# Optimization experiments

Hardware: AMD Instinct MI355X
Metric: run time of the kernel (lower is better)

The kernel has to match this reference:

```python
import jax, jax.numpy as jnp
import numpy as np

B, S, D = 32, 128, 512       # batch, seq_len, input_dim
UNITS = 4096                 # LSTM cell units
PROJ = 512                   # projection_dim
CELL_CLIP = 3.0
PROJ_CLIP = 3.0
W_SCALE = 0.05               # keep gates out of saturation


def hard_sigmoid(x):
    # Keras hard_sigmoid: clip(0.2*x + 0.5, 0, 1)
    return jnp.clip(0.2 * x + 0.5, 0.0, 1.0)


def setup_inputs() -> dict:
    key = jax.random.key(0)
    k = jax.random.split(key, 5)
    x = jax.random.normal(k[0], (B, S, D), dtype=jnp.float32)
    kernel = jax.random.normal(k[1], (D, 4 * UNITS), dtype=jnp.float32) * W_SCALE
    recurrent_kernel = jax.random.normal(k[2], (PROJ, 4 * UNITS), dtype=jnp.float32) * W_SCALE
    bias = jax.random.normal(k[3], (4 * UNITS,), dtype=jnp.float32) * W_SCALE
    # unit_forget_bias: forget-gate slice initialized to ones
    bias = bias.at[UNITS:2 * UNITS].set(1.0)
    projection_kernel = jax.random.normal(k[4], (UNITS, PROJ), dtype=jnp.float32) * W_SCALE
    return {"x": x, "kernel": kernel, "recurrent_kernel": recurrent_kernel,
            "bias": bias, "projection_kernel": projection_kernel}


def reference(x, kernel, recurrent_kernel, bias, projection_kernel):
    # LSTM with cell-state clipping and output projection (ELMo-style).
    # Gate order in fused kernels: [i, f, c, o].
    def step(carry, x_t):
        h, c = carry                              # h: [B,PROJ], c: [B,UNITS]
        z = x_t @ kernel + h @ recurrent_kernel + bias   # [B, 4*UNITS]
        zi, zf, zc, zo = jnp.split(z, 4, axis=-1)
        i = hard_sigmoid(zi)
        f = hard_sigmoid(zf)
        c_new = f * c + i * jnp.tanh(zc)
        o = hard_sigmoid(zo)
        h_new = o * jnp.tanh(c_new)               # uses UNCLIPPED c (matches source)
        c_new = jnp.clip(c_new, -CELL_CLIP, CELL_CLIP)
        h_new = jnp.clip(h_new @ projection_kernel, -PROJ_CLIP, PROJ_CLIP)  # [B,PROJ]
        return (h_new, c_new), h_new

    h0 = jnp.zeros((x.shape[0], PROJ), dtype=x.dtype)
    c0 = jnp.zeros((x.shape[0], UNITS), dtype=x.dtype)
    xs = jnp.transpose(x, (1, 0, 2))              # [S,B,D]
    _, hs = jax.lax.scan(step, (h0, c0), xs)      # hs: [S,B,PROJ]
    return jnp.transpose(hs, (1, 0, 2))           # [B,S,PROJ] (return_sequences)
```

## Files before the change

kernel.cpp:

```cpp
#include <hip/hip_runtime.h>


#define NBLK 256
#define NTHR 512
#define B_   32
#define S_   128
#define D_   512
#define U_   4096
#define PJ   512
#define G4   16384
#define PITC 520
#define LSCALE 2048.0f
#define LINV   4.8828125e-4f

typedef __attribute__((ext_vector_type(8))) _Float16 half8;
typedef __attribute__((ext_vector_type(4))) float floatx4;
typedef __attribute__((ext_vector_type(4))) unsigned int uintx4;

__device__ __forceinline__ void split_h(float f, _Float16& hi, _Float16& lo) {
  _Float16 h = (_Float16)f;
  hi = h;
  lo = (_Float16)((f - (float)h) * LSCALE);
}

__device__ __forceinline__ void stg_dev_u32(unsigned* p, unsigned v) {
  __hip_atomic_store(p, v, __ATOMIC_RELAXED, __HIP_MEMORY_SCOPE_AGENT);
}
__device__ __forceinline__ void store16_sc1(float* p, floatx4 v) {
  asm volatile("global_store_dwordx4 %0, %1, off sc1" :: "v"(p), "v"(v) : "memory");
}
__device__ __forceinline__ uintx4 ld16u_sc1(const unsigned* p) {
  uintx4 r;
  asm volatile("global_load_dwordx4 %0, %1, off sc1\n\ts_waitcnt vmcnt(0)"
               : "=v"(r) : "v"(p) : "memory");
  return r;
}

__global__ __launch_bounds__(NTHR, 2)
void lstm_persistent(const float* __restrict__ x,
                     const float* __restrict__ Wk,
                     const float* __restrict__ R,
                     const float* __restrict__ bias,
                     const float* __restrict__ P,
                     float* __restrict__ out,
                     unsigned* __restrict__ flags1,
                     unsigned* __restrict__ flags2,
                     float* __restrict__ hbuf,
                     float* __restrict__ partial)
{
  __shared__ __align__(16) char smem[100352];
  _Float16* xh_hi = (_Float16*)smem;
  _Float16* xh_lo = xh_hi + B_ * PITC;
  float (*zb)[64][33] = (float (*)[64][33])(smem + 66560);
  float* part_lds = (float*)smem;
  __shared__ float cst[512];
  __shared__ float biasL[64];
  __shared__ _Float16 hph[1024], hpl[1024];
  __shared__ floatx4 redf4[512];

  const int tid  = threadIdx.x;
  const int blk  = blockIdx.x;
  const int lane = tid & 63;
  const int w    = tid >> 6;
  const int ch   = w & 1;
  const int sq   = w >> 1;

  if (tid < 64) {
    int gg = tid >> 4, j = tid & 15;
    biasL[tid] = bias[gg * U_ + blk * 16 + j];
  }
  cst[tid] = 0.f;
  for (int i = tid; i < 1024; i += NTHR) { hph[i] = (_Float16)0.f; hpl[i] = (_Float16)0.f; }

  half8 bhi[2][2][4], blo[2][2][4];
  {
    const int n = lane & 15, q = lane >> 4;
#pragma unroll
    for (int c = 0; c < 2; ++c) {
      const float* Wsrc = c ? R : Wk;
#pragma unroll
      for (int nt = 0; nt < 2; ++nt) {
        int cib  = ch * 32 + nt * 16 + n;
        int gcol = (cib >> 4) * U_ + blk * 16 + (cib & 15);
#pragma unroll
        for (int u = 0; u < 4; ++u) {
          half8 th, tl;
#pragma unroll
          for (int i = 0; i < 8; ++i) {
            int k = (sq * 4 + u) * 32 + q * 8 + i;
            _Float16 hi, lo;
            split_h(Wsrc[(size_t)k * G4 + gcol], hi, lo);
            th[i] = hi; tl[i] = lo;
          }
          bhi[nt][c][u] = th;
          blo[nt][c][u] = tl;
        }
      }
    }
  }

  half8 psh[4], psl[4];
  {
    const int n = lane & 15, q = lane >> 4;
#pragma unroll
    for (int nt = 0; nt < 4; ++nt) {
      half8 th, tl;
#pragma unroll
      for (int i = 0; i < 8; ++i) { th[i] = (_Float16)0.f; tl[i] = (_Float16)0.f; }
      if (q < 2) {
#pragma unroll
        for (int i = 0; i < 8; ++i) {
          int k = q * 8 + i;
          _Float16 hi, lo;
          split_h(P[(size_t)(blk * 16 + k) * PJ + (w * 64 + nt * 16 + n)], hi, lo);
          th[i] = hi; tl[i] = lo;
        }
      }
      psh[nt] = th; psl[nt] = tl;
    }
  }
  __syncthreads();

  const int rb = blk >> 3;
  const int rn = (blk & 7) << 6;
  const int o4 = tid & 15;
  const int gg = tid >> 4;
  const int m_ = lane & 15, q = lane >> 4;

  for (int t = 0; t < S_; ++t) {
    floatx4 acc00 = {0.f, 0.f, 0.f, 0.f};
    floatx4 acc01 = acc00, acc10 = acc00, acc11 = acc00;
    floatx4 accL00 = acc00, accL01 = acc00, accL10 = acc00, accL11 = acc00;

#pragma unroll
    for (int it = 0; it < 4; ++it) {
      int c8 = tid + it * NTHR;
      int b  = c8 >> 6;
      int kg = (c8 & 63) << 3;
      const float* src = x + (size_t)(b * S_ + t) * D_ + kg;
      floatx4 f0 = *(const floatx4*)src;
      floatx4 f1 = *(const floatx4*)(src + 4);
      half8 th, tl; _Float16 hi, lo;
      split_h(f0.x, hi, lo); th[0] = hi; tl[0] = lo;
      split_h(f0.y, hi, lo); th[1] = hi; tl[1] = lo;
      split_h(f0.z, hi, lo); th[2] = hi; tl[2] = lo;
      split_h(f0.w, hi, lo); th[3] = hi; tl[3] = lo;
      split_h(f1.x, hi, lo); th[4] = hi; tl[4] = lo;
      split_h(f1.y, hi, lo); th[5] = hi; tl[5] = lo;
      split_h(f1.z, hi, lo); th[6] = hi; tl[6] = lo;
      split_h(f1.w, hi, lo); th[7] = hi; tl[7] = lo;
      *(half8*)(xh_hi + b * PITC + kg) = th;
      *(half8*)(xh_lo + b * PITC + kg) = tl;
    }
    __syncthreads();

    if (t > 0) {
      const unsigned e = (unsigned)t;
      if (w == 0) {
        for (;;) {
          uintx4 v = ld16u_sc1(flags1 + lane * 4);
          if (__all((int)(v.x >= e && v.y >= e && v.z >= e && v.w >= e))) break;
          __builtin_amdgcn_s_sleep(2);
        }
      }
      __syncthreads();
      {
        const float* pb = partial + (size_t)gg * 16384 + (size_t)rb * PJ + rn + o4 * 4;
        floatx4 r0, r1, r2, r3, r4, r5, r6, r7;
        asm volatile("global_load_dwordx4 %0, %1, off sc1" : "=v"(r0) : "v"(pb)           : "memory");
        asm volatile("global_load_dwordx4 %0, %1, off sc1" : "=v"(r1) : "v"(pb +  524288) : "memory");
        asm volatile("global_load_dwordx4 %0, %1, off sc1" : "=v"(r2) : "v"(pb + 1048576) : "memory");
        asm volatile("global_load_dwordx4 %0, %1, off sc1" : "=v"(r3) : "v"(pb + 1572864) : "memory");
        asm volatile("global_load_dwordx4 %0, %1, off sc1" : "=v"(r4) : "v"(pb + 2097152) : "memory");
        asm volatile("global_load_dwordx4 %0, %1, off sc1" : "=v"(r5) : "v"(pb + 2621440) : "memory");
        asm volatile("global_load_dwordx4 %0, %1, off sc1" : "=v"(r6) : "v"(pb + 3145728) : "memory");
        asm volatile("global_load_dwordx4 %0, %1, off sc1" : "=v"(r7) : "v"(pb + 3670016) : "memory");
        asm volatile("s_waitcnt vmcnt(0)" ::: "memory");
        __builtin_amdgcn_sched_barrier(0);
        floatx4 s = ((r0 + r1) + (r2 + r3)) + ((r4 + r5) + (r6 + r7));
        redf4[gg * 16 + o4] = s;
      }
      __syncthreads();
      if (tid < 16) {
        floatx4 a = redf4[tid];
#pragma unroll
        for (int g2 = 1; g2 < 32; ++g2) a += redf4[g2 * 16 + tid];
        a.x = fminf(fmaxf(a.x, -3.f), 3.f);
        a.y = fminf(fmaxf(a.y, -3.f), 3.f);
        a.z = fminf(fmaxf(a.z, -3.f), 3.f);
        a.w = fminf(fmaxf(a.w, -3.f), 3.f);
        store16_sc1(hbuf + (size_t)t * 16384 + (size_t)rb * PJ + rn + tid * 4, a);
        *(floatx4*)(out + ((size_t)rb * S_ + (t - 1)) * PJ + rn + tid * 4) = a;
      }
      __syncthreads();
      if (tid == 0) stg_dev_u32(flags2 + blk, e);
    }

#pragma unroll
    for (int u = 0; u < 4; ++u) {
      int ko = (sq * 4 + u) * 32 + q * 8;
      half8 ah0 = *(const half8*)(xh_hi + m_ * PITC + ko);
      half8 ah1 = *(const half8*)(xh_hi + (16 + m_) * PITC + ko);
      half8 al0 = *(const half8*)(xh_lo + m_ * PITC + ko);
      half8 al1 = *(const half8*)(xh_lo + (16 + m_) * PITC + ko);
      acc00 = __builtin_amdgcn_mfma_f32_16x16x32_f16(ah0, bhi[0][0][u], acc00, 0, 0, 0);
      acc01 = __builtin_amdgcn_mfma_f32_16x16x32_f16(ah0, bhi[1][0][u], acc01, 0, 0, 0);
      acc10 = __builtin_amdgcn_mfma_f32_16x16x32_f16(ah1, bhi[0][0][u], acc10, 0, 0, 0);
      acc11 = __builtin_amdgcn_mfma_f32_16x16x32_f16(ah1, bhi[1][0][u], acc11, 0, 0, 0);
      accL00 = __builtin_amdgcn_mfma_f32_16x16x32_f16(ah0, blo[0][0][u], accL00, 0, 0, 0);
      accL01 = __builtin_amdgcn_mfma_f32_16x16x32_f16(ah0, blo[1][0][u], accL01, 0, 0, 0);
      accL10 = __builtin_amdgcn_mfma_f32_16x16x32_f16(ah1, blo[0][0][u], accL10, 0, 0, 0);
      accL11 = __builtin_amdgcn_mfma_f32_16x16x32_f16(ah1, blo[1][0][u], accL11, 0, 0, 0);
      accL00 = __builtin_amdgcn_mfma_f32_16x16x32_f16(al0, bhi[0][0][u], accL00, 0, 0, 0);
      accL01 = __builtin_amdgcn_mfma_f32_16x16x32_f16(al0, bhi[1][0][u], accL01, 0, 0, 0);
      accL10 = __builtin_amdgcn_mfma_f32_16x16x32_f16(al1, bhi[0][0][u], accL10, 0, 0, 0);
      accL11 = __builtin_amdgcn_mfma_f32_16x16x32_f16(al1, bhi[1][0][u], accL11, 0, 0, 0);
    }

    if (t > 0) {
      if (w == 0) {
        const unsigned e = (unsigned)t;
        for (;;) {
          uintx4 v = ld16u_sc1(flags2 + lane * 4);
          if (__all((int)(v.x >= e && v.y >= e && v.z >= e && v.w >= e))) break;
          __builtin_amdgcn_s_sleep(2);
        }
      }
    }
    __syncthreads();

    {
      const float* hsl = hbuf + (size_t)t * 16384;
#pragma unroll
      for (int it = 0; it < 4; ++it) {
        int c8 = tid + it * NTHR;
        int b  = c8 >> 6;
        int kg = (c8 & 63) << 3;
        const float* src = hsl + b * PJ + kg;
        floatx4 f0 = *(const floatx4*)src;
        floatx4 f1 = *(const floatx4*)(src + 4);
        half8 th, tl; _Float16 hi, lo;
        split_h(f0.x, hi, lo); th[0] = hi; tl[0] = lo;
        split_h(f0.y, hi, lo); th[1] = hi; tl[1] = lo;
        split_h(f0.z, hi, lo); th[2] = hi; tl[2] = lo;
        split_h(f0.w, hi, lo); th[3] = hi; tl[3] = lo;
        split_h(f1.x, hi, lo); th[4] = hi; tl[4] = lo;
        split_h(f1.y, hi, lo); th[5] = hi; tl[5] = lo;
        split_h(f1.z, hi, lo); th[6] = hi; tl[6] = lo;
        split_h(f1.w, hi, lo); th[7] = hi; tl[7] = lo;
        *(half8*)(xh_hi + b * PITC + kg) = th;
        *(half8*)(xh_lo + b * PITC + kg) = tl;
      }
    }
    __syncthreads();
#pragma unroll
    for (int u = 0; u < 4; ++u) {
      int ko = (sq * 4 + u) * 32 + q * 8;
      half8 ah0 = *(const half8*)(xh_hi + m_ * PITC + ko);
      half8 ah1 = *(const half8*)(xh_hi + (16 + m_) * PITC + ko);
      half8 al0 = *(const half8*)(xh_lo + m_ * PITC + ko);
      half8 al1 = *(const half8*)(xh_lo + (16 + m_) * PITC + ko);
      acc00 = __builtin_amdgcn_mfma_f32_16x16x32_f16(ah0, bhi[0][1][u], acc00, 0, 0, 0);
      acc01 = __builtin_amdgcn_mfma_f32_16x16x32_f16(ah0, bhi[1][1][u], acc01, 0, 0, 0);
      acc10 = __builtin_amdgcn_mfma_f32_16x16x32_f16(ah1, bhi[0][1][u], acc10, 0, 0, 0);
      acc11 = __builtin_amdgcn_mfma_f32_16x16x32_f16(ah1, bhi[1][1][u], acc11, 0, 0, 0);
      accL00 = __builtin_amdgcn_mfma_f32_16x16x32_f16(ah0, blo[0][1][u], accL00, 0, 0, 0);
      accL01 = __builtin_amdgcn_mfma_f32_16x16x32_f16(ah0, blo[1][1][u], accL01, 0, 0, 0);
      accL10 = __builtin_amdgcn_mfma_f32_16x16x32_f16(ah1, blo[0][1][u], accL10, 0, 0, 0);
      accL11 = __builtin_amdgcn_mfma_f32_16x16x32_f16(ah1, blo[1][1][u], accL11, 0, 0, 0);
      accL00 = __builtin_amdgcn_mfma_f32_16x16x32_f16(al0, bhi[0][1][u], accL00, 0, 0, 0);
      accL01 = __builtin_amdgcn_mfma_f32_16x16x32_f16(al0, bhi[1][1][u], accL01, 0, 0, 0);
      accL10 = __builtin_amdgcn_mfma_f32_16x16x32_f16(al1, bhi[0][1][u], accL10, 0, 0, 0);
      accL11 = __builtin_amdgcn_mfma_f32_16x16x32_f16(al1, bhi[1][1][u], accL11, 0, 0, 0);
    }

    {
      int n  = lane & 15;
      int c0 = ch * 32 + n, c1 = ch * 32 + 16 + n;
      int r0 = q * 4,       r1 = 16 + q * 4;
#pragma unroll
      for (int i = 0; i < 4; ++i) {
        zb[sq][c0][r0 + i] = acc00[i] + accL00[i] * LINV;
        zb[sq][c1][r0 + i] = acc01[i] + accL01[i] * LINV;
        zb[sq][c0][r1 + i] = acc10[i] + accL10[i] * LINV;
        zb[sq][c1][r1 + i] = acc11[i] + accL11[i] * LINV;
      }
    }
    __syncthreads();

    {
      int p = tid;
      int b = p >> 4, j = p & 15;
      float zi = zb[0][j][b] + zb[1][j][b] + zb[2][j][b] + zb[3][j][b] + biasL[j];
      float zf = zb[0][16+j][b] + zb[1][16+j][b] + zb[2][16+j][b] + zb[3][16+j][b] + biasL[16+j];
      float zc = zb[0][32+j][b] + zb[1][32+j][b] + zb[2][32+j][b] + zb[3][32+j][b] + biasL[32+j];
      float zo = zb[0][48+j][b] + zb[1][48+j][b] + zb[2][48+j][b] + zb[3][48+j][b] + biasL[48+j];
      float ig = fminf(fmaxf(0.2f * zi + 0.5f, 0.f), 1.f);
      float fg = fminf(fmaxf(0.2f * zf + 0.5f, 0.f), 1.f);
      float og = fminf(fmaxf(0.2f * zo + 0.5f, 0.f), 1.f);
      float cn = fg * cst[p] + ig * tanhf(zc);
      float hp = og * tanhf(cn);
      cst[p] = fminf(fmaxf(cn, -3.f), 3.f);

      _Float16 hh, hl;
      split_h(hp, hh, hl);
      hph[b * 32 + j] = hh;
      hpl[b * 32 + j] = hl;
    }
    __syncthreads();

    {
      floatx4 pa[2][4], pL[2][4];
#pragma unroll
      for (int mt = 0; mt < 2; ++mt)
#pragma unroll
        for (int nt = 0; nt < 4; ++nt) {
          pa[mt][nt] = (floatx4){0.f, 0.f, 0.f, 0.f};
          pL[mt][nt] = (floatx4){0.f, 0.f, 0.f, 0.f};
        }
#pragma unroll
      for (int mt = 0; mt < 2; ++mt) {
        half8 ah = *(const half8*)(hph + (mt * 16 + m_) * 32 + q * 8);
        half8 al = *(const half8*)(hpl + (mt * 16 + m_) * 32 + q * 8);
#pragma unroll
        for (int nt = 0; nt < 4; ++nt) {
          pa[mt][nt] = __builtin_amdgcn_mfma_f32_16x16x32_f16(ah, psh[nt], pa[mt][nt], 0, 0, 0);
          pL[mt][nt] = __builtin_amdgcn_mfma_f32_16x16x32_f16(ah, psl[nt], pL[mt][nt], 0, 0, 0);
          pL[mt][nt] = __builtin_amdgcn_mfma_f32_16x16x32_f16(al, psh[nt], pL[mt][nt], 0, 0, 0);
        }
      }
#pragma unroll
      for (int mt = 0; mt < 2; ++mt)
#pragma unroll
        for (int nt = 0; nt < 4; ++nt)
#pragma unroll
          for (int i = 0; i < 4; ++i) {
            float v = pa[mt][nt][i] + pL[mt][nt][i] * LINV;
            part_lds[(mt * 16 + q * 4 + i) * PJ + w * 64 + nt * 16 + m_] = v;
          }
    }
    __syncthreads();
    {
      const floatx4* srcv = (const floatx4*)part_lds;
      float* dst = partial + (size_t)blk * 16384;
#pragma unroll
      for (int kk = 0; kk < 8; ++kk)
        store16_sc1(dst + kk * 2048 + tid * 4, srcv[kk * 512 + tid]);
    }
    __syncthreads();
    if (tid == 0) stg_dev_u32(flags1 + blk, (unsigned)(t + 1));
  }

  {
    const unsigned e = (unsigned)S_;
    if (w == 0) {
      for (;;) {
        uintx4 v = ld16u_sc1(flags1 + lane * 4);
        if (__all((int)(v.x >= e && v.y >= e && v.z >= e && v.w >= e))) break;
        __builtin_amdgcn_s_sleep(2);
      }
    }
    __syncthreads();
    {
      const float* pb = partial + (size_t)gg * 16384 + (size_t)rb * PJ + rn + o4 * 4;
      floatx4 r0, r1, r2, r3, r4, r5, r6, r7;
      asm volatile("global_load_dwordx4 %0, %1, off sc1" : "=v"(r0) : "v"(pb)           : "memory");
      asm volatile("global_load_dwordx4 %0, %1, off sc1" : "=v"(r1) : "v"(pb +  524288) : "memory");
      asm volatile("global_load_dwordx4 %0, %1, off sc1" : "=v"(r2) : "v"(pb + 1048576) : "memory");
      asm volatile("global_load_dwordx4 %0, %1, off sc1" : "=v"(r3) : "v"(pb + 1572864) : "memory");
      asm volatile("global_load_dwordx4 %0, %1, off sc1" : "=v"(r4) : "v"(pb + 2097152) : "memory");
      asm volatile("global_load_dwordx4 %0, %1, off sc1" : "=v"(r5) : "v"(pb + 2621440) : "memory");
      asm volatile("global_load_dwordx4 %0, %1, off sc1" : "=v"(r6) : "v"(pb + 3145728) : "memory");
      asm volatile("global_load_dwordx4 %0, %1, off sc1" : "=v"(r7) : "v"(pb + 3670016) : "memory");
      asm volatile("s_waitcnt vmcnt(0)" ::: "memory");
      __builtin_amdgcn_sched_barrier(0);
      floatx4 s = ((r0 + r1) + (r2 + r3)) + ((r4 + r5) + (r6 + r7));
      redf4[gg * 16 + o4] = s;
    }
    __syncthreads();
    if (tid < 16) {
      floatx4 a = redf4[tid];
#pragma unroll
      for (int g2 = 1; g2 < 32; ++g2) a += redf4[g2 * 16 + tid];
      a.x = fminf(fmaxf(a.x, -3.f), 3.f);
      a.y = fminf(fmaxf(a.y, -3.f), 3.f);
      a.z = fminf(fmaxf(a.z, -3.f), 3.f);
      a.w = fminf(fmaxf(a.w, -3.f), 3.f);
      *(floatx4*)(out + ((size_t)rb * S_ + (S_ - 1)) * PJ + rn + tid * 4) = a;
    }
  }
}

extern "C" void kernel_launch(void* const* d_in, const int* in_sizes, int n_in,
                              void* d_out, int out_size, void* d_ws, size_t ws_size,
                              hipStream_t stream) {
  const float* x_   = (const float*)d_in[0];
  const float* Wk   = (const float*)d_in[1];
  const float* R_   = (const float*)d_in[2];
  const float* bias = (const float*)d_in[3];
  const float* P_   = (const float*)d_in[4];
  float* out = (float*)d_out;

  unsigned char* ws = (unsigned char*)d_ws;
  unsigned* flags1 = (unsigned*)ws;
  unsigned* flags2 = (unsigned*)(ws + 4096);
  float* hbuf      = (float*)(ws + 16384);
  float* partial   = (float*)(ws + 16384 + 8388608);

  (void)hipMemsetAsync(d_ws, 0, 16384 + 65536, stream);

  lstm_persistent<<<dim3(NBLK), dim3(NTHR), 0, stream>>>(
      x_, Wk, R_, bias, P_, out, flags1, flags2, hbuf, partial);
}
```

Baseline: 2.663 ms.

## Overlap partial-sum reduction with input MFMAs and use fine-grained per-flag spins

Replaces the single-wave flag wait plus block barrier with per-thread checks of only the producer flags each thread depends on, issuing each partial load right after its flag is seen, and interleaves half of the x-projection MFMAs while those loads are in flight. The cross-group reduction becomes two-level (8 then 1) to shorten the serial sum on 16 threads. The published h is pre-split into packed fp16 hi/lo pairs, so consumers skip the split arithmetic when loading h. This adds register pressure and more complex control flow in the critical recurrent path.

```diff
diff --git a/kernel.cpp b/kernel.cpp
--- a/kernel.cpp
+++ b/kernel.cpp
@@ -26,7 +26,13 @@
 __device__ __forceinline__ void stg_dev_u32(unsigned* p, unsigned v) {
   __hip_atomic_store(p, v, __ATOMIC_RELAXED, __HIP_MEMORY_SCOPE_AGENT);
 }
+__device__ __forceinline__ unsigned ldg_dev_u32(const unsigned* p) {
+  return __hip_atomic_load(p, __ATOMIC_RELAXED, __HIP_MEMORY_SCOPE_AGENT);
+}
 __device__ __forceinline__ void store16_sc1(float* p, floatx4 v) {
+  asm volatile("global_store_dwordx4 %0, %1, off sc1" :: "v"(p), "v"(v) : "memory");
+}
+__device__ __forceinline__ void store16u_sc1(unsigned* p, uintx4 v) {
   asm volatile("global_store_dwordx4 %0, %1, off sc1" :: "v"(p), "v"(v) : "memory");
 }
 __device__ __forceinline__ uintx4 ld16u_sc1(const unsigned* p) {
@@ -45,7 +51,7 @@
                      float* __restrict__ out,
                      unsigned* __restrict__ flags1,
                      unsigned* __restrict__ flags2,
-                     float* __restrict__ hbuf,
+                     unsigned* __restrict__ hring,
                      float* __restrict__ partial)
 {
   __shared__ __align__(16) char smem[100352];
@@ -126,6 +132,30 @@
   const int o4 = tid & 15;
   const int gg = tid >> 4;
   const int m_ = lane & 15, q = lane >> 4;
+
+#define B2U(U) do {                                                            \
+    int ko = (sq * 4 + (U)) * 32 + q * 8;                                      \
+    half8 ah0 = *(const half8*)(xh_hi + m_ * PITC + ko);                       \
+    half8 ah1 = *(const half8*)(xh_hi + (16 + m_) * PITC + ko);                \
+    half8 al0 = *(const half8*)(xh_lo + m_ * PITC + ko);                       \
+    half8 al1 = *(const half8*)(xh_lo + (16 + m_) * PITC + ko);                \
+    acc00 = __builtin_amdgcn_mfma_f32_16x16x32_f16(ah0, bhi[0][0][U], acc00, 0, 0, 0); \
+    acc01 = __builtin_amdgcn_mfma_f32_16x16x32_f16(ah0, bhi[1][0][U], acc01, 0, 0, 0); \
+    acc10 = __builtin_amdgcn_mfma_f32_16x16x32_f16(ah1, bhi[0][0][U], acc10, 0, 0, 0); \
+    acc11 = __builtin_amdgcn_mfma_f32_16x16x32_f16(ah1, bhi[1][0][U], acc11, 0, 0, 0); \
+    accL00 = __builtin_amdgcn_mfma_f32_16x16x32_f16(ah0, blo[0][0][U], accL00, 0, 0, 0); \
+    accL01 = __builtin_amdgcn_mfma_f32_16x16x32_f16(ah0, blo[1][0][U], accL01, 0, 0, 0); \
+    accL10 = __builtin_amdgcn_mfma_f32_16x16x32_f16(ah1, blo[0][0][U], accL10, 0, 0, 0); \
+    accL11 = __builtin_amdgcn_mfma_f32_16x16x32_f16(ah1, blo[1][0][U], accL11, 0, 0, 0); \
+    accL00 = __builtin_amdgcn_mfma_f32_16x16x32_f16(al0, bhi[0][0][U], accL00, 0, 0, 0); \
+    accL01 = __builtin_amdgcn_mfma_f32_16x16x32_f16(al0, bhi[1][0][U], accL01, 0, 0, 0); \
+    accL10 = __builtin_amdgcn_mfma_f32_16x16x32_f16(al1, bhi[0][0][U], accL10, 0, 0, 0); \
+    accL11 = __builtin_amdgcn_mfma_f32_16x16x32_f16(al1, bhi[1][0][U], accL11, 0, 0, 0); \
+  } while (0)
+
+#define SPIN1(Rr) for (;;) { unsigned vv = ldg_dev_u32(flags1 + (Rr) * 32 + gg); \
+                             if (__all((int)(vv >= e))) break;                   \
+                             __builtin_amdgcn_s_sleep(2); }
 
   for (int t = 0; t < S_; ++t) {
     floatx4 acc00 = {0.f, 0.f, 0.f, 0.f};
@@ -156,65 +186,72 @@
 
     if (t > 0) {
       const unsigned e = (unsigned)t;
-      if (w == 0) {
-        for (;;) {
-          uintx4 v = ld16u_sc1(flags1 + lane * 4);
-          if (__all((int)(v.x >= e && v.y >= e && v.z >= e && v.w >= e))) break;
-          __builtin_amdgcn_s_sleep(2);
-        }
-      }
+      const float* pbase = partial + (size_t)gg * 16384 + (size_t)rb * PJ + rn + o4 * 4;
+      floatx4 r0, r1, r2, r3, r4, r5, r6, r7;
+      unsigned f0 = ldg_dev_u32(flags1 + gg);
+      unsigned f1 = ldg_dev_u32(flags1 + 32 + gg);
+      unsigned f2 = ldg_dev_u32(flags1 + 64 + gg);
+      unsigned f3 = ldg_dev_u32(flags1 + 96 + gg);
+      unsigned f4 = ldg_dev_u32(flags1 + 128 + gg);
+      unsigned f5 = ldg_dev_u32(flags1 + 160 + gg);
+      unsigned f6 = ldg_dev_u32(flags1 + 192 + gg);
+      unsigned f7 = ldg_dev_u32(flags1 + 224 + gg);
+      bool rdy = (f0 >= e) && (f1 >= e) && (f2 >= e) && (f3 >= e) &&
+                 (f4 >= e) && (f5 >= e) && (f6 >= e) && (f7 >= e);
+      const bool allrdy = __all((int)rdy);
+      if (!allrdy) SPIN1(0)
+      asm volatile("global_load_dwordx4 %0, %1, off sc1" : "=v"(r0) : "v"(pbase)           : "memory");
+      if (!allrdy) SPIN1(1)
+      asm volatile("global_load_dwordx4 %0, %1, off sc1" : "=v"(r1) : "v"(pbase +  524288) : "memory");
+      if (!allrdy) SPIN1(2)
+      asm volatile("global_load_dwordx4 %0, %1, off sc1" : "=v"(r2) : "v"(pbase + 1048576) : "memory");
+      if (!allrdy) SPIN1(3)
+      asm volatile("global_load_dwordx4 %0, %1, off sc1" : "=v"(r3) : "v"(pbase + 1572864) : "memory");
+      if (!allrdy) SPIN1(4)
+      asm volatile("global_load_dwordx4 %0, %1, off sc1" : "=v"(r4) : "v"(pbase + 2097152) : "memory");
+      if (!allrdy) SPIN1(5)
+      asm volatile("global_load_dwordx4 %0, %1, off sc1" : "=v"(r5) : "v"(pbase + 2621440) : "memory");
+      if (!allrdy) SPIN1(6)
+      asm volatile("global_load_dwordx4 %0, %1, off sc1" : "=v"(r6) : "v"(pbase + 3145728) : "memory");
+      if (!allrdy) SPIN1(7)
+      asm volatile("global_load_dwordx4 %0, %1, off sc1" : "=v"(r7) : "v"(pbase + 3670016) : "memory");
+      B2U(0); B2U(1);
+      asm volatile("s_waitcnt vmcnt(0)" ::: "memory");
+      __builtin_amdgcn_sched_barrier(0);
+      floatx4 s = ((r0 + r1) + (r2 + r3)) + ((r4 + r5) + (r6 + r7));
+      redf4[gg * 16 + o4] = s;
       __syncthreads();
-      {
-        const float* pb = partial + (size_t)gg * 16384 + (size_t)rb * PJ + rn + o4 * 4;
-        floatx4 r0, r1, r2, r3, r4, r5, r6, r7;
-        asm volatile("global_load_dwordx4 %0, %1, off sc1" : "=v"(r0) : "v"(pb)           : "memory");
-        asm volatile("global_load_dwordx4 %0, %1, off sc1" : "=v"(r1) : "v"(pb +  524288) : "memory");
-        asm volatile("global_load_dwordx4 %0, %1, off sc1" : "=v"(r2) : "v"(pb + 1048576) : "memory");
-        asm volatile("global_load_dwordx4 %0, %1, off sc1" : "=v"(r3) : "v"(pb + 1572864) : "memory");
-        asm volatile("global_load_dwordx4 %0, %1, off sc1" : "=v"(r4) : "v"(pb + 2097152) : "memory");
-        asm volatile("global_load_dwordx4 %0, %1, off sc1" : "=v"(r5) : "v"(pb + 2621440) : "memory");
-        asm volatile("global_load_dwordx4 %0, %1, off sc1" : "=v"(r6) : "v"(pb + 3145728) : "memory");
-        asm volatile("global_load_dwordx4 %0, %1, off sc1" : "=v"(r7) : "v"(pb + 3670016) : "memory");
-        asm volatile("s_waitcnt vmcnt(0)" ::: "memory");
-        __builtin_amdgcn_sched_barrier(0);
-        floatx4 s = ((r0 + r1) + (r2 + r3)) + ((r4 + r5) + (r6 + r7));
-        redf4[gg * 16 + o4] = s;
+      if (tid < 128) {
+        int ob = tid & 15, g8 = tid >> 4;
+        floatx4 a = redf4[g8 * 16 + ob] + redf4[(g8 + 8) * 16 + ob] +
+                    redf4[(g8 + 16) * 16 + ob] + redf4[(g8 + 24) * 16 + ob];
+        redf4[g8 * 16 + ob] = a;
       }
       __syncthreads();
       if (tid < 16) {
         floatx4 a = redf4[tid];
 #pragma unroll
-        for (int g2 = 1; g2 < 32; ++g2) a += redf4[g2 * 16 + tid];
+        for (int g8 = 1; g8 < 8; ++g8) a += redf4[g8 * 16 + tid];
         a.x = fminf(fmaxf(a.x, -3.f), 3.f);
         a.y = fminf(fmaxf(a.y, -3.f), 3.f);
         a.z = fminf(fmaxf(a.z, -3.f), 3.f);
         a.w = fminf(fmaxf(a.w, -3.f), 3.f);
-        store16_sc1(hbuf + (size_t)t * 16384 + (size_t)rb * PJ + rn + tid * 4, a);
+        uintx4 pk;
+#pragma unroll
+        for (int i = 0; i < 4; ++i) {
+          _Float16 hh, hl;
+          split_h(a[i], hh, hl);
+          pk[i] = (unsigned)__builtin_bit_cast(unsigned short, hh) |
+                  ((unsigned)__builtin_bit_cast(unsigned short, hl) << 16);
+        }
+        store16u_sc1(hring + (size_t)t * 16384 + (size_t)rb * PJ + rn + tid * 4, pk);
         *(floatx4*)(out + ((size_t)rb * S_ + (t - 1)) * PJ + rn + tid * 4) = a;
       }
       __syncthreads();
       if (tid == 0) stg_dev_u32(flags2 + blk, e);
-    }
-
-#pragma unroll
-    for (int u = 0; u < 4; ++u) {
-      int ko = (sq * 4 + u) * 32 + q * 8;
-      half8 ah0 = *(const half8*)(xh_hi + m_ * PITC + ko);
-      half8 ah1 = *(const half8*)(xh_hi + (16 + m_) * PITC + ko);
-      half8 al0 = *(const half8*)(xh_lo + m_ * PITC + ko);
-      half8 al1 = *(const half8*)(xh_lo + (16 + m_) * PITC + ko);
-      acc00 = __builtin_amdgcn_mfma_f32_16x16x32_f16(ah0, bhi[0][0][u], acc00, 0, 0, 0);
-      acc01 = __builtin_amdgcn_mfma_f32_16x16x32_f16(ah0, bhi[1][0][u], acc01, 0, 0, 0);
-      acc10 = __builtin_amdgcn_mfma_f32_16x16x32_f16(ah1, bhi[0][0][u], acc10, 0, 0, 0);
-      acc11 = __builtin_amdgcn_mfma_f32_16x16x32_f16(ah1, bhi[1][0][u], acc11, 0, 0, 0);
-      accL00 = __builtin_amdgcn_mfma_f32_16x16x32_f16(ah0, blo[0][0][u], accL00, 0, 0, 0);
-      accL01 = __builtin_amdgcn_mfma_f32_16x16x32_f16(ah0, blo[1][0][u], accL01, 0, 0, 0);
-      accL10 = __builtin_amdgcn_mfma_f32_16x16x32_f16(ah1, blo[0][0][u], accL10, 0, 0, 0);
-      accL11 = __builtin_amdgcn_mfma_f32_16x16x32_f16(ah1, blo[1][0][u], accL11, 0, 0, 0);
-      accL00 = __builtin_amdgcn_mfma_f32_16x16x32_f16(al0, bhi[0][0][u], accL00, 0, 0, 0);
-      accL01 = __builtin_amdgcn_mfma_f32_16x16x32_f16(al0, bhi[1][0][u], accL01, 0, 0, 0);
-      accL10 = __builtin_amdgcn_mfma_f32_16x16x32_f16(al1, bhi[0][0][u], accL10, 0, 0, 0);
-      accL11 = __builtin_amdgcn_mfma_f32_16x16x32_f16(al1, bhi[1][0][u], accL11, 0, 0, 0);
+      B2U(2); B2U(3);
+    } else {
+      B2U(0); B2U(1); B2U(2); B2U(3);
     }
 
     if (t > 0) {
@@ -230,24 +267,32 @@
     __syncthreads();
 
     {
-      const float* hsl = hbuf + (size_t)t * 16384;
+      const unsigned* hsl = hring + (size_t)t * 16384;
 #pragma unroll
       for (int it = 0; it < 4; ++it) {
         int c8 = tid + it * NTHR;
         int b  = c8 >> 6;
         int kg = (c8 & 63) << 3;
-        const float* src = hsl + b * PJ + kg;
-        floatx4 f0 = *(const floatx4*)src;
-        floatx4 f1 = *(const floatx4*)(src + 4);
-        half8 th, tl; _Float16 hi, lo;
-        split_h(f0.x, hi, lo); th[0] = hi; tl[0] = lo;
-        split_h(f0.y, hi, lo); th[1] = hi; tl[1] = lo;
-        split_h(f0.z, hi, lo); th[2] = hi; tl[2] = lo;
-        split_h(f0.w, hi, lo); th[3] = hi; tl[3] = lo;
-        split_h(f1.x, hi, lo); th[4] = hi; tl[4] = lo;
-        split_h(f1.y, hi, lo); th[5] = hi; tl[5] = lo;
-        split_h(f1.z, hi, lo); th[6] = hi; tl[6] = lo;
-        split_h(f1.w, hi, lo); th[7] = hi; tl[7] = lo;
+        const unsigned* src = hsl + b * PJ + kg;
+        uintx4 v0 = *(const uintx4*)src;
+        uintx4 v1 = *(const uintx4*)(src + 4);
+        half8 th, tl;
+        th[0] = __builtin_bit_cast(_Float16, (unsigned short)(v0.x & 0xffffu));
+        tl[0] = __builtin_bit_cast(_Float16, (unsigned short)(v0.x >> 16));
+        th[1] = __builtin_bit_cast(_Float16, (unsigned short)(v0.y & 0xffffu));
+        tl[1] = __builtin_bit_cast(_Float16, (unsigned short)(v0.y >> 16));
+        th[2] = __builtin_bit_cast(_Float16, (unsigned short)(v0.z & 0xffffu));
+        tl[2] = __builtin_bit_cast(_Float16, (unsigned short)(v0.z >> 16));
+        th[3] = __builtin_bit_cast(_Float16, (unsigned short)(v0.w & 0xffffu));
+        tl[3] = __builtin_bit_cast(_Float16, (unsigned short)(v0.w >> 16));
+        th[4] = __builtin_bit_cast(_Float16, (unsigned short)(v1.x & 0xffffu));
+        tl[4] = __builtin_bit_cast(_Float16, (unsigned short)(v1.x >> 16));
+        th[5] = __builtin_bit_cast(_Float16, (unsigned short)(v1.y & 0xffffu));
+        tl[5] = __builtin_bit_cast(_Float16, (unsigned short)(v1.y >> 16));
+        th[6] = __builtin_bit_cast(_Float16, (unsigned short)(v1.z & 0xffffu));
+        tl[6] = __builtin_bit_cast(_Float16, (unsigned short)(v1.z >> 16));
+        th[7] = __builtin_bit_cast(_Float16, (unsigned short)(v1.w & 0xffffu));
+        tl[7] = __builtin_bit_cast(_Float16, (unsigned short)(v1.w >> 16));
         *(half8*)(xh_hi + b * PITC + kg) = th;
         *(half8*)(xh_lo + b * PITC + kg) = tl;
       }
@@ -404,11 +449,11 @@
   unsigned char* ws = (unsigned char*)d_ws;
   unsigned* flags1 = (unsigned*)ws;
   unsigned* flags2 = (unsigned*)(ws + 4096);
-  float* hbuf      = (float*)(ws + 16384);
+  unsigned* hring  = (unsigned*)(ws + 16384);
   float* partial   = (float*)(ws + 16384 + 8388608);
 
   (void)hipMemsetAsync(d_ws, 0, 16384 + 65536, stream);
 
   lstm_persistent<<<dim3(NBLK), dim3(NTHR), 0, stream>>>(
-      x_, Wk, R_, bias, P_, out, flags1, flags2, hbuf, partial);
-}
+      x_, Wk, R_, bias, P_, out, flags1, flags2, hring, partial);
+}
```

New measurement: 2.580 ms (median of 2 runs). -3.1%, faster.
